# Optimization experiments

Measured on AMD Instinct MI355X. Metric: run time of the kernel, lower is better.

Reference implementation:

```python
import jax, jax.numpy as jnp
import numpy as np

B, N, F_IN = 32, 1024, 64   # batch, num_nodes, diffusion_size[0]
K = 3                        # expansion_step
H = 2                        # num_heads
HID, RAW, OUT, CLS = 128, 128, 128, 2
D1, D2 = 128, 128            # diffusion_size[1], diffusion_size[2]
CAT = D1 + RAW               # concat dim fed to attention (h || h_prime) = 256


def setup_inputs() -> dict:
    key = jax.random.key(0)
    ks = jax.random.split(key, 40)
    g = lambda i, shape: jax.random.normal(ks[i], shape, dtype=jnp.float32) * 0.05
    inp = {
        'X': jax.random.normal(ks[0], (B, N, F_IN), dtype=jnp.float32),
        'A': jax.random.uniform(ks[1], (B, N, N), dtype=jnp.float32),
        # transition tensors / mixing weights (only the 2 layers used in forward)
        'T': g(2, (2, K, N, N)),
        'theta': jnp.full((2, K), 1.0 / K, dtype=jnp.float32),
        # raw feature projection
        'W_raw': g(3, (F_IN, RAW)), 'b_raw': jnp.zeros((RAW,), jnp.float32),
        # diffusion layer linears
        'Wd0': g(4, (F_IN, D1)), 'bd0': jnp.zeros((D1,), jnp.float32),
        'Wd1': g(5, (D1, D2)),   'bd1': jnp.zeros((D2,), jnp.float32),
        # final classifier
        'W_fin': g(6, (OUT, CLS)), 'b_fin': jnp.zeros((CLS,), jnp.float32),
    }
    # two CatMultiAttn blocks: q/k/v projections (CAT->HID), out proj (HID->OUT)
    i = 7
    for l in range(2):
        for nm in ('q', 'k', 'v'):
            inp[f'W{nm}{l}'] = g(i, (CAT, HID)); i += 1
            inp[f'b{nm}{l}'] = jnp.zeros((HID,), jnp.float32)
        inp[f'Wo{l}'] = g(i, (HID, OUT)); i += 1
        inp[f'bo{l}'] = jnp.zeros((OUT,), jnp.float32)
    return inp


def _diffusion(theta_l, T_l, h, A, W, b):
    # Q = sum_k theta_k * T_k  (generalized graph diffusion transition)
    Q = jnp.einsum('k,kij->ij', theta_l, T_l)          # [N,N]
    S = Q[None, :, :] * A                               # [B,N,N] mask by adjacency
    z = jnp.einsum('bij,bjf->bif', S, h)                # diffuse features
    return jax.nn.relu(z @ W + b)


def _cat_attn(h, hp, Wq, bq, Wk, bk, Wv, bv, Wo, bo):
    # concatenate diffused + embedding features, multi-head self-attn over nodes
    x = jnp.concatenate([h, hp], axis=-1)               # [B,N,CAT]
    b, n, _ = x.shape
    q = (x @ Wq + bq).reshape(b, n, H, HID // H)
    k = (x @ Wk + bk).reshape(b, n, H, HID // H)
    v = (x @ Wv + bv).reshape(b, n, H, HID // H)
    scale = jnp.asarray(1.0 / np.sqrt(HID // H), x.dtype)
    s = jnp.einsum('bnhd,bmhd->bhnm', q, k) * scale     # [B,H,N,N]
    p = jax.nn.softmax(s, axis=-1)
    ctx = jnp.einsum('bhnm,bmhd->bnhd', p, v).reshape(b, n, HID)
    return jax.nn.relu(ctx @ Wo + bo)


def reference(X, A, T, theta, W_raw, b_raw, Wd0, bd0, Wd1, bd1,
              W_fin, b_fin,
              Wq0, bq0, Wk0, bk0, Wv0, bv0, Wo0, bo0,
              Wq1, bq1, Wk1, bk1, Wv1, bv1, Wo1, bo1):
    theta_soft = jax.nn.softmax(theta, axis=-1)         # [2,K]
    h_prime = X @ W_raw + b_raw                          # [B,N,RAW]
    # layer 0
    h = _diffusion(theta_soft[0], T[0], X, A, Wd0, bd0)  # [B,N,D1]
    h_prime = _cat_attn(h, h_prime, Wq0, bq0, Wk0, bk0, Wv0, bv0, Wo0, bo0)
    # layer 1 (residual fusion)
    h = _diffusion(theta_soft[1], T[1], h, A, Wd1, bd1)  # [B,N,D2]
    h_prime = h_prime + _cat_attn(h, h_prime, Wq1, bq1, Wk1, bk1, Wv1, bv1, Wo1, bo1)
    return h_prime @ W_fin + b_fin                       # [B,N,CLS]
```

## Files before the change

kernel.cpp:

```cpp
#include <hip/hip_runtime.h>
#include <hip/hip_bf16.h>

typedef __hip_bfloat16 bf16;
typedef __attribute__((ext_vector_type(8))) short s8b;
typedef __attribute__((ext_vector_type(4))) short s4b;
typedef __attribute__((ext_vector_type(4))) float f4;

#define BB   32
#define NN   1024
#define FIN  64
#define HEADS 2
#define DH   64
#define HIDD 128
#define SZQ  ((size_t)BB * NN * HIDD)

__device__ __forceinline__ ushort f2bf(float x) {
    bf16 h = __float2bfloat16(x);
    return *(ushort*)&h;
}
__device__ __forceinline__ float bfbits2f(ushort h) {
    union { uint u; float f; } c; c.u = (uint)h << 16; return c.f;
}
__device__ __forceinline__ uint pk_bf16(float lo, float hi) {
    return (uint)f2bf(lo) | ((uint)f2bf(hi) << 16);
}
union U8 { short s[8]; s8b v; };
union U4 { short s[4]; s4b v; };

__global__ __launch_bounds__(256) void build_q_kernel(const float* __restrict__ T,
                                                      const float* __restrict__ theta,
                                                      int layer, float* __restrict__ Q) {
    float t0 = theta[layer * 3 + 0];
    float t1 = theta[layer * 3 + 1];
    float t2 = theta[layer * 3 + 2];
    float m  = fmaxf(t0, fmaxf(t1, t2));
    float e0 = expf(t0 - m), e1 = expf(t1 - m), e2 = expf(t2 - m);
    float inv = 1.0f / (e0 + e1 + e2);
    e0 *= inv; e1 *= inv; e2 *= inv;
    size_t idx = (size_t)blockIdx.x * blockDim.x + threadIdx.x;
    const float* Tl = T + (size_t)layer * 3 * NN * NN;
    Q[idx] = e0 * Tl[idx]
           + e1 * Tl[idx + (size_t)NN * NN]
           + e2 * Tl[idx + (size_t)2 * NN * NN];
}

__global__ __launch_bounds__(256) void prep_w_kernel(
        const float* __restrict__ raw, const float* __restrict__ d0,
        const float* __restrict__ d1,
        const float* __restrict__ q0, const float* __restrict__ k0,
        const float* __restrict__ v0, const float* __restrict__ o0,
        const float* __restrict__ q1, const float* __restrict__ k1,
        const float* __restrict__ v1, const float* __restrict__ o1,
        ushort* __restrict__ hi, ushort* __restrict__ lo) {
    int id = blockIdx.x * 256 + threadIdx.x;
    const float* src; int K, off;
    if      (id <   8192) { src = raw; K =  64; off = 0; }
    else if (id <  16384) { src = d0;  K =  64; off = 8192; }
    else if (id <  32768) { src = d1;  K = 128; off = 16384; }
    else if (id <  65536) { src = q0;  K = 256; off = 32768; }
    else if (id <  98304) { src = k0;  K = 256; off = 65536; }
    else if (id < 131072) { src = v0;  K = 256; off = 98304; }
    else if (id < 147456) { src = o0;  K = 128; off = 131072; }
    else if (id < 180224) { src = q1;  K = 256; off = 147456; }
    else if (id < 212992) { src = k1;  K = 256; off = 180224; }
    else if (id < 245760) { src = v1;  K = 256; off = 212992; }
    else                  { src = o1;  K = 128; off = 245760; }
    int il = id - off;
    int k = il >> 7, c = il & 127;
    float w = src[il];
    ushort h = f2bf(w);
    hi[off + c * K + k] = h;
    lo[off + c * K + k] = f2bf(w - bfbits2f(h));
}

__global__ __launch_bounds__(256) void transpose_split64_kernel(const float* __restrict__ X,
                                                                ushort* __restrict__ hiT,
                                                                ushort* __restrict__ loT) {
    __shared__ float tile[64][65];
    const int b  = blockIdx.x >> 4;
    const int n0 = (blockIdx.x & 15) * 64;
    const int t  = threadIdx.x;
    {
        int nl = t >> 2, f0 = (t & 3) * 16;
        const float* xp = X + ((size_t)b * NN + n0 + nl) * 64 + f0;
#pragma unroll
        for (int i = 0; i < 16; i += 4)
            *(float4*)&tile[nl][f0 + i] = *(const float4*)(xp + i);
    }
    __syncthreads();
    {
        int f = t >> 2, n1 = (t & 3) * 16;
        U8 h0, h1, l0, l1;
#pragma unroll
        for (int i = 0; i < 16; i++) {
            float v = tile[n1 + i][f];
            ushort hh = f2bf(v);
            ushort ll = f2bf(v - bfbits2f(hh));
            if (i < 8) { h0.s[i] = (short)hh; l0.s[i] = (short)ll; }
            else       { h1.s[i - 8] = (short)hh; l1.s[i - 8] = (short)ll; }
        }
        size_t gb = ((size_t)b * 64 + f) * NN + n0 + n1;
        *(s8b*)&hiT[gb]     = h0.v;  *(s8b*)&hiT[gb + 8] = h1.v;
        *(s8b*)&loT[gb]     = l0.v;  *(s8b*)&loT[gb + 8] = l1.v;
    }
}

template<int F>
__global__ __launch_bounds__(256) void diffusion_mfma_kernel(const float* __restrict__ Q,
                                                             const float* __restrict__ A,
                                                             const ushort* __restrict__ hT_hi,
                                                             const ushort* __restrict__ hT_lo,
                                                             float* __restrict__ z) {
    constexpr int SS  = 72;
    constexpr int NT  = F / 16;
    constexpr int TPW = (2 * NT) / 4;
    __shared__ short Shi[32][SS], Slo[32][SS];
    __shared__ short Hhi[F][SS],  Hlo[F][SS];

    const int b    = blockIdx.x >> 5;
    const int i0   = (blockIdx.x & 31) * 32;
    const int t    = threadIdx.x;
    const int w    = t >> 6, lane = t & 63;
    const int quad = lane >> 4, c = lane & 15;
    const int mt   = w & 1;
    const int n0t  = (w >> 1) * TPW;

    f4 acc[TPW];
#pragma unroll
    for (int i = 0; i < TPW; i++) acc[i] = (f4){0.f, 0.f, 0.f, 0.f};

    for (int j0 = 0; j0 < NN; j0 += 64) {
        __syncthreads();
        {
            int il = t >> 3, jc = (t & 7) * 8;
            const float* ap = A + ((size_t)b * NN + (i0 + il)) * NN + j0 + jc;
            const float* qp = Q + (size_t)(i0 + il) * NN + j0 + jc;
            float4 a0 = *(const float4*)ap,       a1 = *(const float4*)(ap + 4);
            float4 q0 = *(const float4*)qp,       q1 = *(const float4*)(qp + 4);
            float sv[8] = {a0.x*q0.x, a0.y*q0.y, a0.z*q0.z, a0.w*q0.w,
                           a1.x*q1.x, a1.y*q1.y, a1.z*q1.z, a1.w*q1.w};
            U8 hi, lo;
#pragma unroll
            for (int i = 0; i < 8; i++) {
                ushort hh = f2bf(sv[i]);
                hi.s[i] = (short)hh;
                lo.s[i] = (short)f2bf(sv[i] - bfbits2f(hh));
            }
            *(s8b*)&Shi[il][jc] = hi.v;
            *(s8b*)&Slo[il][jc] = lo.v;
        }
        {
            constexpr int TPR = 256 / F;
            constexpr int CPT = 64 / TPR;
            int fr = t / TPR, cg = (t % TPR) * CPT;
            const ushort* gh = hT_hi + ((size_t)b * F + fr) * NN + j0 + cg;
            const ushort* gl = hT_lo + ((size_t)b * F + fr) * NN + j0 + cg;
#pragma unroll
            for (int i = 0; i < CPT; i += 8) {
                *(s8b*)&Hhi[fr][cg + i] = *(const s8b*)(gh + i);
                *(s8b*)&Hlo[fr][cg + i] = *(const s8b*)(gl + i);
            }
        }
        __syncthreads();

#pragma unroll
        for (int ks = 0; ks < 2; ks++) {
            s8b ahi = *(const s8b*)&Shi[mt * 16 + c][ks * 32 + quad * 8];
            s8b alo = *(const s8b*)&Slo[mt * 16 + c][ks * 32 + quad * 8];
#pragma unroll
            for (int tt = 0; tt < TPW; tt++) {
                const int nt = n0t + tt;
                s8b bhi = *(const s8b*)&Hhi[nt * 16 + c][ks * 32 + quad * 8];
                s8b blo = *(const s8b*)&Hlo[nt * 16 + c][ks * 32 + quad * 8];
                acc[tt] = __builtin_amdgcn_mfma_f32_16x16x32_bf16(ahi, bhi, acc[tt], 0, 0, 0);
                acc[tt] = __builtin_amdgcn_mfma_f32_16x16x32_bf16(alo, bhi, acc[tt], 0, 0, 0);
                acc[tt] = __builtin_amdgcn_mfma_f32_16x16x32_bf16(ahi, blo, acc[tt], 0, 0, 0);
            }
        }
    }
#pragma unroll
    for (int tt = 0; tt < TPW; tt++)
#pragma unroll
        for (int r = 0; r < 4; r++)
            z[((size_t)b * NN + i0 + mt * 16 + quad * 4 + r) * F + (n0t + tt) * 16 + c] = acc[tt][r];
}

template<int K1, int K2, int CB, bool RELU, bool RESID, int OMODE>
__global__ __launch_bounds__(256) void dense_mfma_kernel(
        const float* __restrict__ in1, const float* __restrict__ in2,
        const ushort* __restrict__ WT_hi, const ushort* __restrict__ WT_lo,
        const float* __restrict__ bias, const float* __restrict__ biask,
        const float* __restrict__ biasv,
        float* __restrict__ out, ushort* __restrict__ outq,
        ushort* __restrict__ hiT, ushort* __restrict__ loT) {
    constexpr int KD  = K1 + K2;
    constexpr int NKT = KD / 32;
    constexpr int NCT = CB / 16;
    __shared__ short Xhi[64][40], Xlo[64][40];
    __shared__ short Whi[CB][40], Wlo[CB][40];

    const int r0 = blockIdx.x * 64;
    const int c0 = blockIdx.y * CB;
    const int t  = threadIdx.x;
    const int w  = t >> 6, lane = t & 63;
    const int quad = lane >> 4, c = lane & 15;

    f4 acc[NCT];
#pragma unroll
    for (int i = 0; i < NCT; i++) acc[i] = (f4){0.f, 0.f, 0.f, 0.f};

    for (int kt = 0; kt < NKT; kt++) {
        const int k0 = kt * 32;
        __syncthreads();
        {
            int row = t >> 2, kk = (t & 3) * 8;
            int g = r0 + row;
            const float* p;
            if (K2 > 0) {
                int k = k0 + kk;
                p = (k < K1) ? (in1 + (size_t)g * K1 + k)
                             : (in2 + (size_t)g * K2 + (k - K1));
            } else {
                p = in1 + (size_t)g * K1 + k0 + kk;
            }
            float4 a = *(const float4*)p, bq = *(const float4*)(p + 4);
            float sv[8] = {a.x, a.y, a.z, a.w, bq.x, bq.y, bq.z, bq.w};
            U8 hi, lo;
#pragma unroll
            for (int i = 0; i < 8; i++) {
                ushort hh = f2bf(sv[i]);
                hi.s[i] = (short)hh;
                lo.s[i] = (short)f2bf(sv[i] - bfbits2f(hh));
            }
            *(s8b*)&Xhi[row][kk] = hi.v;
            *(s8b*)&Xlo[row][kk] = lo.v;
        }
        {
#pragma unroll
            for (int p = 0; p < CB / 64; p++) {
                int cc = p * 64 + (t >> 2), kk = (t & 3) * 8;
                size_t gsrc = (size_t)(c0 + cc) * KD + k0 + kk;
                *(s8b*)&Whi[cc][kk] = *(const s8b*)&WT_hi[gsrc];
                *(s8b*)&Wlo[cc][kk] = *(const s8b*)&WT_lo[gsrc];
            }
        }
        __syncthreads();

        s8b ah = *(const s8b*)&Xhi[16 * w + c][quad * 8];
        s8b al = *(const s8b*)&Xlo[16 * w + c][quad * 8];
#pragma unroll
        for (int ct = 0; ct < NCT; ct++) {
            s8b bh = *(const s8b*)&Whi[ct * 16 + c][quad * 8];
            s8b bl = *(const s8b*)&Wlo[ct * 16 + c][quad * 8];
            acc[ct] = __builtin_amdgcn_mfma_f32_16x16x32_bf16(ah, bh, acc[ct], 0, 0, 0);
            acc[ct] = __builtin_amdgcn_mfma_f32_16x16x32_bf16(al, bh, acc[ct], 0, 0, 0);
            acc[ct] = __builtin_amdgcn_mfma_f32_16x16x32_bf16(ah, bl, acc[ct], 0, 0, 0);
        }
    }

    const int row_g0 = r0 + 16 * w + quad * 4;
#pragma unroll
    for (int ct = 0; ct < NCT; ct++) {
        const int col = c0 + ct * 16 + c;
        if (OMODE == 1) {
            int tensor = col >> 7, cc2 = col & 127;
            float bv = (tensor == 0 ? bias : tensor == 1 ? biask : biasv)[cc2];
            int head = cc2 >> 6, d = cc2 & 63;
            int b = row_g0 >> 10, n = row_g0 & 1023;
            ushort* dst = outq + (size_t)tensor * SZQ
                        + (((size_t)b * HEADS + head) * NN + n) * 64 + d;
#pragma unroll
            for (int r = 0; r < 4; r++) dst[(size_t)r * 64] = f2bf(acc[ct][r] + bv);
        } else {
            float bv = bias[col];
            float vv[4];
#pragma unroll
            for (int r = 0; r < 4; r++) {
                float v = acc[ct][r] + bv;
                if (RELU) v = fmaxf(v, 0.f);
                size_t o = (size_t)(row_g0 + r) * 128 + col;
                if (RESID) v += out[o];
                out[o] = v;
                vv[r] = v;
            }
            if (OMODE == 2) {
                int b = row_g0 >> 10, n = row_g0 & 1023;
                U4 ph, pl;
#pragma unroll
                for (int r = 0; r < 4; r++) {
                    ushort hh = f2bf(vv[r]);
                    ph.s[r] = (short)hh;
                    pl.s[r] = (short)f2bf(vv[r] - bfbits2f(hh));
                }
                size_t tb = ((size_t)b * 128 + col) * NN + n;
                *(s4b*)&hiT[tb] = ph.v;
                *(s4b*)&loT[tb] = pl.v;
            }
        }
    }
}

__global__ __launch_bounds__(256) void attn_mfma_kernel(const ushort* __restrict__ q,
                                                        const ushort* __restrict__ k,
                                                        const ushort* __restrict__ v,
                                                        float* __restrict__ ctx) {
    __shared__ short Ks[64][68];
    __shared__ short Vt[64][68];

    const int bh = blockIdx.x >> 4;
    const int n0 = (blockIdx.x & 15) * 64;
    const int b  = bh >> 1, h = bh & 1;
    const int t  = threadIdx.x;
    const int w  = t >> 6;
    const int lane = t & 63;
    const int quad = lane >> 4, c = lane & 15;
    const size_t kvbase = (size_t)bh * NN * 64;
    const float scale = 0.125f;

    s8b qf0, qf1;
    {
        const ushort* qrow = q + kvbase + (size_t)(n0 + 16 * w + c) * 64;
        qf0 = *(const s8b*)(qrow + quad * 8);
        qf1 = *(const s8b*)(qrow + 32 + quad * 8);
    }

    f4 O[4];
#pragma unroll
    for (int i = 0; i < 4; i++) O[i] = (f4){0.f, 0.f, 0.f, 0.f};
    float m_i = -1e30f, l_i = 0.f;

    for (int kt0 = 0; kt0 < NN; kt0 += 64) {
        __syncthreads();
        {
            int key = t >> 2, d0 = (t & 3) * 16;
            const ushort* kr = k + kvbase + (size_t)(kt0 + key) * 64 + d0;
            s8b k0 = *(const s8b*)kr, k1 = *(const s8b*)(kr + 8);
            *(s4b*)&Ks[key][d0]      = __builtin_shufflevector(k0, k0, 0, 1, 2, 3);
            *(s4b*)&Ks[key][d0 + 4]  = __builtin_shufflevector(k0, k0, 4, 5, 6, 7);
            *(s4b*)&Ks[key][d0 + 8]  = __builtin_shufflevector(k1, k1, 0, 1, 2, 3);
            *(s4b*)&Ks[key][d0 + 12] = __builtin_shufflevector(k1, k1, 4, 5, 6, 7);
            int vkey = t & 63, vd0 = (t >> 6) * 16;
            const ushort* vr = v + kvbase + (size_t)(kt0 + vkey) * 64 + vd0;
            s8b v0 = *(const s8b*)vr, v1 = *(const s8b*)(vr + 8);
#pragma unroll
            for (int i = 0; i < 8; i++) {
                Vt[vd0 + i][vkey]     = v0[i];
                Vt[vd0 + 8 + i][vkey] = v1[i];
            }
        }
        __syncthreads();

#pragma unroll
        for (int u = 0; u < 2; u++) {
            const int kb = u * 32;
            f4 sa = (f4){0.f, 0.f, 0.f, 0.f};
            f4 sb = (f4){0.f, 0.f, 0.f, 0.f};
#pragma unroll
            for (int ch = 0; ch < 2; ch++) {
                const short* pa = &Ks[kb + c][ch * 32 + quad * 8];
                const short* pb = &Ks[kb + 16 + c][ch * 32 + quad * 8];
                s4b a0 = *(const s4b*)pa, a1 = *(const s4b*)(pa + 4);
                s4b b0 = *(const s4b*)pb, b1 = *(const s4b*)(pb + 4);
                s8b ka = __builtin_shufflevector(a0, a1, 0, 1, 2, 3, 4, 5, 6, 7);
                s8b kB = __builtin_shufflevector(b0, b1, 0, 1, 2, 3, 4, 5, 6, 7);
                s8b qf = ch ? qf1 : qf0;
                sa = __builtin_amdgcn_mfma_f32_16x16x32_bf16(ka, qf, sa, 0, 0, 0);
                sb = __builtin_amdgcn_mfma_f32_16x16x32_bf16(kB, qf, sb, 0, 0, 0);
            }
            float pv[8];
#pragma unroll
            for (int r = 0; r < 4; r++) { pv[r] = sa[r] * scale; pv[4 + r] = sb[r] * scale; }
            float mx = pv[0];
#pragma unroll
            for (int j = 1; j < 8; j++) mx = fmaxf(mx, pv[j]);
            mx = fmaxf(mx, __shfl_xor(mx, 16));
            mx = fmaxf(mx, __shfl_xor(mx, 32));
            float newm  = fmaxf(m_i, mx);
            float alpha = __expf(m_i - newm);
            float ps = 0.f;
#pragma unroll
            for (int j = 0; j < 8; j++) { pv[j] = __expf(pv[j] - newm); ps += pv[j]; }
            ps += __shfl_xor(ps, 16);
            ps += __shfl_xor(ps, 32);
            l_i = l_i * alpha + ps;
            m_i = newm;
#pragma unroll
            for (int dt = 0; dt < 4; dt++)
#pragma unroll
                for (int r = 0; r < 4; r++) O[dt][r] *= alpha;

            uint Da01 = pk_bf16(pv[0], pv[1]), Da23 = pk_bf16(pv[2], pv[3]);
            uint Db01 = pk_bf16(pv[4], pv[5]), Db23 = pk_bf16(pv[6], pv[7]);
            int addr0 = ((((2 * quad) & 3) << 4) | c) << 2;
            int addr1 = ((((2 * quad + 1) & 3) << 4) | c) << 2;
            int A01_0 = __builtin_amdgcn_ds_bpermute(addr0, (int)Da01);
            int A23_0 = __builtin_amdgcn_ds_bpermute(addr0, (int)Da23);
            int B01_0 = __builtin_amdgcn_ds_bpermute(addr0, (int)Db01);
            int B23_0 = __builtin_amdgcn_ds_bpermute(addr0, (int)Db23);
            int A01_1 = __builtin_amdgcn_ds_bpermute(addr1, (int)Da01);
            int A23_1 = __builtin_amdgcn_ds_bpermute(addr1, (int)Da23);
            int B01_1 = __builtin_amdgcn_ds_bpermute(addr1, (int)Db01);
            int B23_1 = __builtin_amdgcn_ds_bpermute(addr1, (int)Db23);
            int tsel = quad >> 1;
            union { int i[4]; s8b s; } pf;
            pf.i[0] = tsel ? B01_0 : A01_0;
            pf.i[1] = tsel ? B23_0 : A23_0;
            pf.i[2] = tsel ? B01_1 : A01_1;
            pf.i[3] = tsel ? B23_1 : A23_1;

#pragma unroll
            for (int dt = 0; dt < 4; dt++) {
                const short* pvp = &Vt[16 * dt + c][kb + quad * 8];
                s4b v0 = *(const s4b*)pvp, v1 = *(const s4b*)(pvp + 4);
                s8b vf = __builtin_shufflevector(v0, v1, 0, 1, 2, 3, 4, 5, 6, 7);
                O[dt] = __builtin_amdgcn_mfma_f32_16x16x32_bf16(vf, pf.s, O[dt], 0, 0, 0);
            }
        }
    }

    float inv = 1.0f / l_i;
    float* crow = ctx + ((size_t)b * NN + n0 + 16 * w + c) * HIDD + h * DH;
#pragma unroll
    for (int dt = 0; dt < 4; dt++)
#pragma unroll
        for (int r = 0; r < 4; r++)
            crow[16 * dt + 4 * quad + r] = O[dt][r] * inv;
}

__global__ __launch_bounds__(256) void final_kernel(const float* __restrict__ hp,
                                                    const float* __restrict__ Wf,
                                                    const float* __restrict__ bf_,
                                                    float* __restrict__ out) {
    int id = blockIdx.x * blockDim.x + threadIdx.x;
    int r = id >> 1, c = id & 1;
    const float* row = hp + (size_t)r * 128;
    float acc = bf_[c];
    for (int kk = 0; kk < 128; kk++) acc += row[kk] * Wf[kk * 2 + c];
    out[id] = acc;
}

extern "C" void kernel_launch(void* const* d_in, const int* in_sizes, int n_in,
                              void* d_out, int out_size, void* d_ws, size_t ws_size,
                              hipStream_t stream) {
    (void)in_sizes; (void)n_in; (void)out_size; (void)ws_size;
    const float* X     = (const float*)d_in[0];
    const float* A     = (const float*)d_in[1];
    const float* T     = (const float*)d_in[2];
    const float* theta = (const float*)d_in[3];
    const float* W_raw = (const float*)d_in[4];
    const float* b_raw = (const float*)d_in[5];
    const float* Wd0   = (const float*)d_in[6];
    const float* bd0   = (const float*)d_in[7];
    const float* Wd1   = (const float*)d_in[8];
    const float* bd1   = (const float*)d_in[9];
    const float* W_fin = (const float*)d_in[10];
    const float* b_fin = (const float*)d_in[11];
    const float* Wq0 = (const float*)d_in[12]; const float* bq0 = (const float*)d_in[13];
    const float* Wk0 = (const float*)d_in[14]; const float* bk0 = (const float*)d_in[15];
    const float* Wv0 = (const float*)d_in[16]; const float* bv0 = (const float*)d_in[17];
    const float* Wo0 = (const float*)d_in[18]; const float* bo0 = (const float*)d_in[19];
    const float* Wq1 = (const float*)d_in[20]; const float* bq1 = (const float*)d_in[21];
    const float* Wk1 = (const float*)d_in[22]; const float* bk1 = (const float*)d_in[23];
    const float* Wv1 = (const float*)d_in[24]; const float* bv1 = (const float*)d_in[25];
    const float* Wo1 = (const float*)d_in[26]; const float* bo1 = (const float*)d_in[27];

    float* ws   = (float*)d_ws;
    const size_t SZ = (size_t)BB * NN * HIDD;
    float* Qbuf = ws;
    float* hp   = Qbuf + (size_t)NN * NN;
    float* h    = hp + SZ;
    float* z    = h + SZ;
    ushort* qb  = (ushort*)(z + SZ);
    ushort* kb  = qb + SZ;
    ushort* vb  = kb + SZ;
    ushort* XT_hi = vb + SZ;
    ushort* XT_lo = XT_hi + SZ / 2;
    ushort* hT_hi = XT_lo + SZ / 2;
    ushort* hT_lo = hT_hi + SZ;
    ushort* WT_hi = hT_lo + SZ;
    ushort* WT_lo = WT_hi + 262144;

    const int OFF_RAW = 0, OFF_D0 = 8192, OFF_D1 = 16384, OFF_QKV0 = 32768,
              OFF_O0 = 131072, OFF_QKV1 = 147456, OFF_O1 = 245760;

    const int attnGrid = BB * HEADS * (NN / 64);
    const int diffGrid = BB * (NN / 32);
    const dim3 dg1(512, 1), dg2(512, 2);

    prep_w_kernel<<<1024, 256, 0, stream>>>(W_raw, Wd0, Wd1, Wq0, Wk0, Wv0, Wo0,
                                            Wq1, Wk1, Wv1, Wo1, WT_hi, WT_lo);
    build_q_kernel<<<(NN * NN) / 256, 256, 0, stream>>>(T, theta, 0, Qbuf);
    transpose_split64_kernel<<<BB * (NN / 64), 256, 0, stream>>>(X, XT_hi, XT_lo);

    dense_mfma_kernel<64, 0, 128, false, false, 0><<<dg1, 256, 0, stream>>>(
        X, nullptr, WT_hi + OFF_RAW, WT_lo + OFF_RAW, b_raw, nullptr, nullptr,
        hp, nullptr, nullptr, nullptr);
    diffusion_mfma_kernel<64><<<diffGrid, 256, 0, stream>>>(Qbuf, A, XT_hi, XT_lo, z);
    dense_mfma_kernel<64, 0, 128, true, false, 2><<<dg1, 256, 0, stream>>>(
        z, nullptr, WT_hi + OFF_D0, WT_lo + OFF_D0, bd0, nullptr, nullptr,
        h, nullptr, hT_hi, hT_lo);
    dense_mfma_kernel<128, 128, 192, false, false, 1><<<dg2, 256, 0, stream>>>(
        h, hp, WT_hi + OFF_QKV0, WT_lo + OFF_QKV0, bq0, bk0, bv0,
        nullptr, qb, nullptr, nullptr);
    attn_mfma_kernel<<<attnGrid, 256, 0, stream>>>(qb, kb, vb, z);
    dense_mfma_kernel<128, 0, 128, true, false, 0><<<dg1, 256, 0, stream>>>(
        z, nullptr, WT_hi + OFF_O0, WT_lo + OFF_O0, bo0, nullptr, nullptr,
        hp, nullptr, nullptr, nullptr);

    build_q_kernel<<<(NN * NN) / 256, 256, 0, stream>>>(T, theta, 1, Qbuf);
    diffusion_mfma_kernel<128><<<diffGrid, 256, 0, stream>>>(Qbuf, A, hT_hi, hT_lo, z);
    dense_mfma_kernel<128, 0, 128, true, false, 0><<<dg1, 256, 0, stream>>>(
        z, nullptr, WT_hi + OFF_D1, WT_lo + OFF_D1, bd1, nullptr, nullptr,
        h, nullptr, nullptr, nullptr);
    dense_mfma_kernel<128, 128, 192, false, false, 1><<<dg2, 256, 0, stream>>>(
        h, hp, WT_hi + OFF_QKV1, WT_lo + OFF_QKV1, bq1, bk1, bv1,
        nullptr, qb, nullptr, nullptr);
    attn_mfma_kernel<<<attnGrid, 256, 0, stream>>>(qb, kb, vb, z);
    dense_mfma_kernel<128, 0, 128, true, true, 0><<<dg1, 256, 0, stream>>>(
        z, nullptr, WT_hi + OFF_O1, WT_lo + OFF_O1, bo1, nullptr, nullptr,
        hp, nullptr, nullptr, nullptr);

    final_kernel<<<(BB * NN * 2) / 256, 256, 0, stream>>>(hp, W_fin, b_fin, (float*)d_out);
}
```

Measured before the change: 601.6 us.

## Enlarge diffusion tile to 64 rows with register prefetch and bf16-split Q

The diffusion kernel now processes 64 output rows per 512-thread block, which halves how often each batch's h tile is reloaded. It prefetches the next A and h chunks into registers while the MFMAs run on the current tile. Q is precomputed as bf16 hi/lo pairs, so the kernel reads 4 bytes per element instead of 4 floats of Q. The trade-offs are more registers and LDS per block, and a tiny precision change from rounding Q to hi+lo bf16.

```diff
diff --git a/kernel.cpp b/kernel.cpp
--- a/kernel.cpp
+++ b/kernel.cpp
@@ -26,10 +26,13 @@
 }
 union U8 { short s[8]; s8b v; };
 union U4 { short s[4]; s4b v; };
-
-__global__ __launch_bounds__(256) void build_q_kernel(const float* __restrict__ T,
-                                                      const float* __restrict__ theta,
-                                                      int layer, float* __restrict__ Q) {
+union UQ { ushort u[8]; s8b v; };
+
+__global__ __launch_bounds__(256) void build_q_split_kernel(const float* __restrict__ T,
+                                                            const float* __restrict__ theta,
+                                                            int layer,
+                                                            ushort* __restrict__ Qhi,
+                                                            ushort* __restrict__ Qlo) {
     float t0 = theta[layer * 3 + 0];
     float t1 = theta[layer * 3 + 1];
     float t2 = theta[layer * 3 + 2];
@@ -37,11 +40,20 @@
     float e0 = expf(t0 - m), e1 = expf(t1 - m), e2 = expf(t2 - m);
     float inv = 1.0f / (e0 + e1 + e2);
     e0 *= inv; e1 *= inv; e2 *= inv;
-    size_t idx = (size_t)blockIdx.x * blockDim.x + threadIdx.x;
+    size_t base = ((size_t)blockIdx.x * 256 + threadIdx.x) * 8;
     const float* Tl = T + (size_t)layer * 3 * NN * NN;
-    Q[idx] = e0 * Tl[idx]
-           + e1 * Tl[idx + (size_t)NN * NN]
-           + e2 * Tl[idx + (size_t)2 * NN * NN];
+    U8 hi, lo;
+#pragma unroll
+    for (int i = 0; i < 8; i++) {
+        float q = e0 * Tl[base + i]
+                + e1 * Tl[base + i + (size_t)NN * NN]
+                + e2 * Tl[base + i + (size_t)2 * NN * NN];
+        ushort hh = f2bf(q);
+        hi.s[i] = (short)hh;
+        lo.s[i] = (short)f2bf(q - bfbits2f(hh));
+    }
+    *(s8b*)&Qhi[base] = hi.v;
+    *(s8b*)&Qlo[base] = lo.v;
 }
 
 __global__ __launch_bounds__(256) void prep_w_kernel(
@@ -106,59 +118,79 @@
 }
 
 template<int F>
-__global__ __launch_bounds__(256) void diffusion_mfma_kernel(const float* __restrict__ Q,
-                                                             const float* __restrict__ A,
-                                                             const ushort* __restrict__ hT_hi,
-                                                             const ushort* __restrict__ hT_lo,
-                                                             float* __restrict__ z) {
+__global__ __launch_bounds__(512, 4) void diffusion_mfma_kernel(
+        const ushort* __restrict__ Qhi, const ushort* __restrict__ Qlo,
+        const float* __restrict__ A,
+        const ushort* __restrict__ hT_hi, const ushort* __restrict__ hT_lo,
+        float* __restrict__ z) {
     constexpr int SS  = 72;
     constexpr int NT  = F / 16;
-    constexpr int TPW = (2 * NT) / 4;
-    __shared__ short Shi[32][SS], Slo[32][SS];
+    constexpr int TPW = NT / 2;
+    __shared__ short Shi[64][SS], Slo[64][SS];
     __shared__ short Hhi[F][SS],  Hlo[F][SS];
 
-    const int b    = blockIdx.x >> 5;
-    const int i0   = (blockIdx.x & 31) * 32;
-    const int t    = threadIdx.x;
-    const int w    = t >> 6, lane = t & 63;
+    const int b  = blockIdx.x >> 4;
+    const int i0 = (blockIdx.x & 15) * 64;
+    const int t  = threadIdx.x;
+    const int w  = t >> 6, lane = t & 63;
     const int quad = lane >> 4, c = lane & 15;
-    const int mt   = w & 1;
-    const int n0t  = (w >> 1) * TPW;
+    const int mt = w >> 1, nh = w & 1;
+
+    const int srow = t >> 3, scol = (t & 7) * 8;
+    const float*  Ap = A   + ((size_t)b * NN + i0 + srow) * NN + scol;
+    const ushort* Qh = Qhi + (size_t)(i0 + srow) * NN + scol;
+    const ushort* Ql = Qlo + (size_t)(i0 + srow) * NN + scol;
+    constexpr int HTR = 512 / F;
+    constexpr int HJ  = 64 / HTR;
+    constexpr int HV  = HJ / 8;
+    const int hrow = t / HTR, hcol = (t % HTR) * HJ;
+    const ushort* Hh = hT_hi + ((size_t)b * F + hrow) * NN + hcol;
+    const ushort* Hl = hT_lo + ((size_t)b * F + hrow) * NN + hcol;
 
     f4 acc[TPW];
 #pragma unroll
     for (int i = 0; i < TPW; i++) acc[i] = (f4){0.f, 0.f, 0.f, 0.f};
 
+    float4 a0 = *(const float4*)Ap, a1 = *(const float4*)(Ap + 4);
+    s8b hhv[HV], hlv[HV];
+#pragma unroll
+    for (int vv = 0; vv < HV; vv++) {
+        hhv[vv] = *(const s8b*)(Hh + 8 * vv);
+        hlv[vv] = *(const s8b*)(Hl + 8 * vv);
+    }
+
+#pragma unroll 1
     for (int j0 = 0; j0 < NN; j0 += 64) {
+        UQ qh, ql;
+        qh.v = *(const s8b*)(Qh + j0);
+        ql.v = *(const s8b*)(Ql + j0);
         __syncthreads();
         {
-            int il = t >> 3, jc = (t & 7) * 8;
-            const float* ap = A + ((size_t)b * NN + (i0 + il)) * NN + j0 + jc;
-            const float* qp = Q + (size_t)(i0 + il) * NN + j0 + jc;
-            float4 a0 = *(const float4*)ap,       a1 = *(const float4*)(ap + 4);
-            float4 q0 = *(const float4*)qp,       q1 = *(const float4*)(qp + 4);
-            float sv[8] = {a0.x*q0.x, a0.y*q0.y, a0.z*q0.z, a0.w*q0.w,
-                           a1.x*q1.x, a1.y*q1.y, a1.z*q1.z, a1.w*q1.w};
+            float av[8] = {a0.x, a0.y, a0.z, a0.w, a1.x, a1.y, a1.z, a1.w};
             U8 hi, lo;
 #pragma unroll
             for (int i = 0; i < 8; i++) {
-                ushort hh = f2bf(sv[i]);
-                hi.s[i] = (short)hh;
-                lo.s[i] = (short)f2bf(sv[i] - bfbits2f(hh));
-            }
-            *(s8b*)&Shi[il][jc] = hi.v;
-            *(s8b*)&Slo[il][jc] = lo.v;
-        }
-        {
-            constexpr int TPR = 256 / F;
-            constexpr int CPT = 64 / TPR;
-            int fr = t / TPR, cg = (t % TPR) * CPT;
-            const ushort* gh = hT_hi + ((size_t)b * F + fr) * NN + j0 + cg;
-            const ushort* gl = hT_lo + ((size_t)b * F + fr) * NN + j0 + cg;
-#pragma unroll
-            for (int i = 0; i < CPT; i += 8) {
-                *(s8b*)&Hhi[fr][cg + i] = *(const s8b*)(gh + i);
-                *(s8b*)&Hlo[fr][cg + i] = *(const s8b*)(gl + i);
+                float q = bfbits2f(qh.u[i]) + bfbits2f(ql.u[i]);
+                float s = q * av[i];
+                ushort hb = f2bf(s);
+                hi.s[i] = (short)hb;
+                lo.s[i] = (short)f2bf(s - bfbits2f(hb));
+            }
+            *(s8b*)&Shi[srow][scol] = hi.v;
+            *(s8b*)&Slo[srow][scol] = lo.v;
+#pragma unroll
+            for (int vv = 0; vv < HV; vv++) {
+                *(s8b*)&Hhi[hrow][hcol + 8 * vv] = hhv[vv];
+                *(s8b*)&Hlo[hrow][hcol + 8 * vv] = hlv[vv];
+            }
+        }
+        if (j0 + 64 < NN) {
+            a0 = *(const float4*)(Ap + j0 + 64);
+            a1 = *(const float4*)(Ap + j0 + 68);
+#pragma unroll
+            for (int vv = 0; vv < HV; vv++) {
+                hhv[vv] = *(const s8b*)(Hh + j0 + 64 + 8 * vv);
+                hlv[vv] = *(const s8b*)(Hl + j0 + 64 + 8 * vv);
             }
         }
         __syncthreads();
@@ -169,7 +201,7 @@
             s8b alo = *(const s8b*)&Slo[mt * 16 + c][ks * 32 + quad * 8];
 #pragma unroll
             for (int tt = 0; tt < TPW; tt++) {
-                const int nt = n0t + tt;
+                const int nt = nh * TPW + tt;
                 s8b bhi = *(const s8b*)&Hhi[nt * 16 + c][ks * 32 + quad * 8];
                 s8b blo = *(const s8b*)&Hlo[nt * 16 + c][ks * 32 + quad * 8];
                 acc[tt] = __builtin_amdgcn_mfma_f32_16x16x32_bf16(ahi, bhi, acc[tt], 0, 0, 0);
@@ -182,7 +214,7 @@
     for (int tt = 0; tt < TPW; tt++)
 #pragma unroll
         for (int r = 0; r < 4; r++)
-            z[((size_t)b * NN + i0 + mt * 16 + quad * 4 + r) * F + (n0t + tt) * 16 + c] = acc[tt][r];
+            z[((size_t)b * NN + i0 + mt * 16 + quad * 4 + r) * F + (nh * TPW + tt) * 16 + c] = acc[tt][r];
 }
 
 template<int K1, int K2, int CB, bool RELU, bool RESID, int OMODE>
@@ -466,8 +498,9 @@
 
     float* ws   = (float*)d_ws;
     const size_t SZ = (size_t)BB * NN * HIDD;
-    float* Qbuf = ws;
-    float* hp   = Qbuf + (size_t)NN * NN;
+    ushort* Qhi = (ushort*)ws;
+    ushort* Qlo = Qhi + (size_t)NN * NN;
+    float* hp   = ws + (size_t)NN * NN;
     float* h    = hp + SZ;
     float* z    = h + SZ;
     ushort* qb  = (ushort*)(z + SZ);
@@ -484,18 +517,18 @@
               OFF_O0 = 131072, OFF_QKV1 = 147456, OFF_O1 = 245760;
 
     const int attnGrid = BB * HEADS * (NN / 64);
-    const int diffGrid = BB * (NN / 32);
+    const int diffGrid = BB * (NN / 64);
     const dim3 dg1(512, 1), dg2(512, 2);
 
     prep_w_kernel<<<1024, 256, 0, stream>>>(W_raw, Wd0, Wd1, Wq0, Wk0, Wv0, Wo0,
                                             Wq1, Wk1, Wv1, Wo1, WT_hi, WT_lo);
-    build_q_kernel<<<(NN * NN) / 256, 256, 0, stream>>>(T, theta, 0, Qbuf);
+    build_q_split_kernel<<<(NN * NN) / (256 * 8), 256, 0, stream>>>(T, theta, 0, Qhi, Qlo);
     transpose_split64_kernel<<<BB * (NN / 64), 256, 0, stream>>>(X, XT_hi, XT_lo);
 
     dense_mfma_kernel<64, 0, 128, false, false, 0><<<dg1, 256, 0, stream>>>(
         X, nullptr, WT_hi + OFF_RAW, WT_lo + OFF_RAW, b_raw, nullptr, nullptr,
         hp, nullptr, nullptr, nullptr);
-    diffusion_mfma_kernel<64><<<diffGrid, 256, 0, stream>>>(Qbuf, A, XT_hi, XT_lo, z);
+    diffusion_mfma_kernel<64><<<diffGrid, 512, 0, stream>>>(Qhi, Qlo, A, XT_hi, XT_lo, z);
     dense_mfma_kernel<64, 0, 128, true, false, 2><<<dg1, 256, 0, stream>>>(
         z, nullptr, WT_hi + OFF_D0, WT_lo + OFF_D0, bd0, nullptr, nullptr,
         h, nullptr, hT_hi, hT_lo);
@@ -507,8 +540,8 @@
         z, nullptr, WT_hi + OFF_O0, WT_lo + OFF_O0, bo0, nullptr, nullptr,
         hp, nullptr, nullptr, nullptr);
 
-    build_q_kernel<<<(NN * NN) / 256, 256, 0, stream>>>(T, theta, 1, Qbuf);
-    diffusion_mfma_kernel<128><<<diffGrid, 256, 0, stream>>>(Qbuf, A, hT_hi, hT_lo, z);
+    build_q_split_kernel<<<(NN * NN) / (256 * 8), 256, 0, stream>>>(T, theta, 1, Qhi, Qlo);
+    diffusion_mfma_kernel<128><<<diffGrid, 512, 0, stream>>>(Qhi, Qlo, A, hT_hi, hT_lo, z);
     dense_mfma_kernel<128, 0, 128, true, false, 0><<<dg1, 256, 0, stream>>>(
         z, nullptr, WT_hi + OFF_D1, WT_lo + OFF_D1, bd1, nullptr, nullptr,
         h, nullptr, nullptr, nullptr);
```

Result: faster. 569.9 us (-5.3%).
